# Kernel tuning notes

Measured on AMD Instinct MI355X. Metric: run time of the kernel, lower is better.

Reference implementation:

```python
import jax, jax.numpy as jnp
import numpy as np

NEG = -10000.0
START_ID, END_ID, PAD_ID = 0, 1, 2
B, S, T = 512, 512, 128


def setup_inputs() -> dict:
    key = jax.random.key(0)
    k1, k2, k3, k4 = jax.random.split(key, 4)
    x = jax.random.normal(k1, (B, S, T), dtype=jnp.float32)
    tags = jax.random.randint(k2, (B, S), 0, T)
    # prefix-ones mask; lengths in [1, S-2] so the gather at mask.sum(1) is in-range
    lengths = jax.random.randint(k3, (B,), 1, S - 1)
    mask = (jnp.arange(S)[None, :] < lengths[:, None]).astype(jnp.float32)
    # torch xavier_normal_ on (T, T): std = sqrt(2 / (T + T))
    std = (2.0 / (T + T)) ** 0.5
    transition = std * jax.random.normal(k4, (T, T), dtype=jnp.float32)
    return {"x": x, "tags": tags, "mask": mask, "transition": transition}


def _crf_forward(x, mask, transition):
    # forward algorithm: log partition function, shape (B,)
    b, s, t = x.shape
    alpha0 = jnp.full((b, t), NEG, dtype=x.dtype).at[:, START_ID].set(0.0)

    def step(alpha, inp):
        x_t, m_t = inp  # (B,T), (B,)
        # scores[b, next, prev] = alpha[b, prev] + x_t[b, next] + transition[next, prev]
        scores = alpha[:, None, :] + x_t[:, :, None] + transition[None, :, :]
        new = jax.scipy.special.logsumexp(scores, axis=2)  # (B,T)
        m = m_t[:, None]
        return new * m + alpha * (1.0 - m), None

    alpha, _ = jax.lax.scan(step, alpha0, (jnp.swapaxes(x, 0, 1), jnp.swapaxes(mask, 0, 1)))
    return jax.scipy.special.logsumexp(alpha + transition[END_ID], axis=1)


def _crf_score(x, tags, mask, transition):
    # gold path score, shape (B,) — emission at t is paired with tags[:, t+1]
    b, s, t = x.shape
    em = jnp.take_along_axis(x[:, : s - 1], tags[:, 1:s, None], axis=2)[..., 0]  # (B,S-1)
    tr = transition[tags[:, 1:s], tags[:, : s - 1]]  # (B,S-1)
    score = jnp.sum((em + tr) * mask[:, : s - 1], axis=1)
    last_idx = mask.sum(axis=1).astype(jnp.int32)  # (B,)
    last_tag = jnp.take_along_axis(tags, last_idx[:, None], axis=1)[:, 0]
    return score + transition[END_ID, last_tag]


def reference(x, tags, mask, transition):
    fwd_score = _crf_forward(x, mask, transition)
    gold_score = _crf_score(x, tags, mask, transition)
    return jnp.mean(fwd_score - gold_score)
```

## Files before the change

kernel.cpp:

```cpp
#include <hip/hip_runtime.h>

#define NTAG 128
#define SEQ 512
#define NBATCH 512
#define END_ID 1

typedef _Float16 h2 __attribute__((ext_vector_type(2)));
typedef __fp16 fp16x2 __attribute__((ext_vector_type(2)));
typedef uint u32x32 __attribute__((ext_vector_type(32)));

#define LOG2E 1.4426950408889634f
#define LN2   0.6931471805599453f

__device__ __forceinline__ float bcast0(float v) {
  return __int_as_float(__builtin_amdgcn_readfirstlane(__float_as_int(v)));
}
__device__ __forceinline__ uint pack2(float a, float b) {
  fp16x2 h = __builtin_amdgcn_cvt_pkrtz(a, b);
  return __builtin_bit_cast(uint, h);
}
__device__ __forceinline__ h2 as_h2(uint u) { return __builtin_bit_cast(h2, u); }

__device__ __forceinline__ float fast_exp2(float x) {
#if __has_builtin(__builtin_amdgcn_exp2f)
  return __builtin_amdgcn_exp2f(x);
#else
  return exp2f(x);
#endif
}
__device__ __forceinline__ float fast_log2(float x) {
#if __has_builtin(__builtin_amdgcn_logf)
  return __builtin_amdgcn_logf(x);
#else
  return log2f(x);
#endif
}

#if __has_builtin(__builtin_amdgcn_fdot2)
#define FDOT2(pu, eu, acc) acc = __builtin_amdgcn_fdot2(as_h2(pu), as_h2(eu), acc, false)
#else
#define FDOT2(pu, eu, acc) do { h2 _p = as_h2(pu), _e = as_h2(eu); \
  acc = fmaf((float)_p.x, (float)_e.x, fmaf((float)_p.y, (float)_e.y, acc)); } while (0)
#endif

#define RL(v, l) ((uint)__builtin_amdgcn_readlane((int)(v), (l)))
#define EL(c) ((c) < 32 ? eL0[(c)] : eL1[(c) - 32])
#define EH(c) ((c) < 32 ? eH0[(c)] : eH1[(c) - 32])

__global__ __launch_bounds__(64, 1) void crf_kernel(
    const float* __restrict__ x,
    const int*   __restrict__ tags,
    const float* __restrict__ mask,
    const float* __restrict__ trans,
    float* __restrict__ ws)
{
  const int b    = blockIdx.x;
  const int lane = threadIdx.x;

  const float* xb   = x    + (size_t)b * SEQ * NTAG;
  const float* mrow = mask + (size_t)b * SEQ;
  const int*   trow = tags + (size_t)b * SEQ;

  float msum = 0.f;
  #pragma unroll
  for (int i = 0; i < SEQ / 64; ++i) msum += mrow[lane + i * 64];
  #pragma unroll
  for (int off = 1; off < 64; off <<= 1) msum += __shfl_xor(msum, off);
  const int len = (int)msum;

  u32x32 eL0, eL1, eH0, eH1;
  {
    const float4* r0 = (const float4*)(trans + (size_t)(2 * lane) * NTAG);
    const float4* r1 = (const float4*)(trans + (size_t)(2 * lane + 1) * NTAG);
    #pragma unroll
    for (int k4 = 0; k4 < 16; ++k4) {
      float4 lo = r0[k4], hi = r1[k4];
      eL0[2 * k4 + 0] = pack2(fast_exp2(lo.x * LOG2E), fast_exp2(lo.y * LOG2E));
      eL0[2 * k4 + 1] = pack2(fast_exp2(lo.z * LOG2E), fast_exp2(lo.w * LOG2E));
      eH0[2 * k4 + 0] = pack2(fast_exp2(hi.x * LOG2E), fast_exp2(hi.y * LOG2E));
      eH0[2 * k4 + 1] = pack2(fast_exp2(hi.z * LOG2E), fast_exp2(hi.w * LOG2E));
    }
    #pragma unroll
    for (int k4 = 16; k4 < 32; ++k4) {
      float4 lo = r0[k4], hi = r1[k4];
      eL1[2 * (k4 - 16) + 0] = pack2(fast_exp2(lo.x * LOG2E), fast_exp2(lo.y * LOG2E));
      eL1[2 * (k4 - 16) + 1] = pack2(fast_exp2(lo.z * LOG2E), fast_exp2(lo.w * LOG2E));
      eH1[2 * (k4 - 16) + 0] = pack2(fast_exp2(hi.x * LOG2E), fast_exp2(hi.y * LOG2E));
      eH1[2 * (k4 - 16) + 1] = pack2(fast_exp2(hi.z * LOG2E), fast_exp2(hi.w * LOG2E));
    }
  }

  float A_lo = (lane == 0) ? 0.f : -14427.f;
  float A_hi = -14427.f;

  const float2* xrow = (const float2*)xb;
  float2 xf0 = xrow[0 * 64 + lane];
  float2 xf1 = xrow[1 * 64 + lane];
  float2 xf2 = xrow[2 * 64 + lane];
  float2 xf3 = xrow[3 * 64 + lane];

#define CRF_STEP(XF, S)                                                       \
  {                                                                           \
    const int g = t + (S);                                                    \
    const float M = bcast0(A_lo);                                             \
    const uint pk = pack2(fminf(fast_exp2(A_lo - M), 60000.f),                \
                          fminf(fast_exp2(A_hi - M), 60000.f));               \
    const float2 xt = XF;                                                     \
    XF = xrow[(size_t)min(g + 4, len) * 64 + lane];  \
    float qL0 = 0.f, qL1 = 0.f, qL2 = 0.f, qL3 = 0.f;                         \
    float qH0 = 0.f, qH1 = 0.f, qH2 = 0.f, qH3 = 0.f;                         \
    _Pragma("unroll")                                                         \
    for (int gg = 0; gg < 64; gg += 8) {                                      \
      const uint s0 = RL(pk, gg + 0), s1 = RL(pk, gg + 1);                    \
      const uint s2 = RL(pk, gg + 2), s3 = RL(pk, gg + 3);                    \
      const uint s4 = RL(pk, gg + 4), s5 = RL(pk, gg + 5);                    \
      const uint s6 = RL(pk, gg + 6), s7 = RL(pk, gg + 7);                    \
      FDOT2(s0, EL(gg + 0), qL0); FDOT2(s0, EH(gg + 0), qH0);                 \
      FDOT2(s1, EL(gg + 1), qL1); FDOT2(s1, EH(gg + 1), qH1);                 \
      FDOT2(s2, EL(gg + 2), qL2); FDOT2(s2, EH(gg + 2), qH2);                 \
      FDOT2(s3, EL(gg + 3), qL3); FDOT2(s3, EH(gg + 3), qH3);                 \
      FDOT2(s4, EL(gg + 4), qL0); FDOT2(s4, EH(gg + 4), qH0);                 \
      FDOT2(s5, EL(gg + 5), qL1); FDOT2(s5, EH(gg + 5), qH1);                 \
      FDOT2(s6, EL(gg + 6), qL2); FDOT2(s6, EH(gg + 6), qH2);                 \
      FDOT2(s7, EL(gg + 7), qL3); FDOT2(s7, EH(gg + 7), qH3);                 \
    }                                                                         \
    const float qL = (qL0 + qL1) + (qL2 + qL3);                               \
    const float qH = (qH0 + qH1) + (qH2 + qH3);                               \
    const float nL = fmaf(xt.x, LOG2E, M + fast_log2(qL));                    \
    const float nH = fmaf(xt.y, LOG2E, M + fast_log2(qH));                    \
    const bool act = (g < len);                                               \
    A_lo = act ? nL : A_lo;                                                   \
    A_hi = act ? nH : A_hi;                                                   \
  }

  for (int t = 0; t < len; t += 4) {
    CRF_STEP(xf0, 0)
    CRF_STEP(xf1, 1)
    CRF_STEP(xf2, 2)
    CRF_STEP(xf3, 3)
  }
#undef CRF_STEP

  const float a_lo = A_lo * LN2;
  const float a_hi = A_hi * LN2;

  const float2 te = ((const float2*)(trans + END_ID * NTAG))[lane];
  const float v_lo = a_lo + te.x;
  const float v_hi = a_hi + te.y;
  float m2 = fmaxf(v_lo, v_hi);
  #pragma unroll
  for (int off = 1; off < 64; off <<= 1) m2 = fmaxf(m2, __shfl_xor(m2, off));
  float s = fast_exp2((v_lo - m2) * LOG2E) + fast_exp2((v_hi - m2) * LOG2E);
  #pragma unroll
  for (int off = 1; off < 64; off <<= 1) s += __shfl_xor(s, off);
  const float fwd = m2 + fast_log2(s) * LN2;

  float g = 0.f;
  for (int i = lane; i < len; i += 64) {
    const int tn = trow[i + 1];
    const int tp = trow[i];
    g += xb[(size_t)i * NTAG + tn] + trans[tn * NTAG + tp];
  }
  #pragma unroll
  for (int off = 1; off < 64; off <<= 1) g += __shfl_xor(g, off);

  if (lane == 0) {
    const float gold = g + trans[END_ID * NTAG + trow[len]];
    ws[b] = fwd - gold;
  }
}

__global__ void reduce_kernel(const float* __restrict__ ws, float* __restrict__ out) {
  __shared__ float sm[8];
  const int tid = threadIdx.x;
  float v = ws[tid];
  #pragma unroll
  for (int off = 1; off < 64; off <<= 1) v += __shfl_xor(v, off);
  if ((tid & 63) == 0) sm[tid >> 6] = v;
  __syncthreads();
  if (tid == 0) {
    float s = 0.f;
    #pragma unroll
    for (int w = 0; w < 8; ++w) s += sm[w];
    out[0] = s * (1.0f / 512.0f);
  }
}

extern "C" void kernel_launch(void* const* d_in, const int* in_sizes, int n_in,
                              void* d_out, int out_size, void* d_ws, size_t ws_size,
                              hipStream_t stream) {
  const float* x     = (const float*)d_in[0];
  const int*   tags  = (const int*)d_in[1];
  const float* mask  = (const float*)d_in[2];
  const float* trans = (const float*)d_in[3];
  float*       ws    = (float*)d_ws;

  crf_kernel<<<NBATCH, 64, 0, stream>>>(x, tags, mask, trans, ws);
  reduce_kernel<<<1, 512, 0, stream>>>(ws, (float*)d_out);
}
```

Baseline: 389.3 us.

## Split CRF forward recursion across two waves with LDS exchange and linear-domain scaling

Result: slower. 465.6 us (+19.6%).

```diff
diff --git a/kernel.cpp b/kernel.cpp
--- a/kernel.cpp
+++ b/kernel.cpp
@@ -7,14 +7,10 @@
 
 typedef _Float16 h2 __attribute__((ext_vector_type(2)));
 typedef __fp16 fp16x2 __attribute__((ext_vector_type(2)));
-typedef uint u32x32 __attribute__((ext_vector_type(32)));
 
 #define LOG2E 1.4426950408889634f
 #define LN2   0.6931471805599453f
 
-__device__ __forceinline__ float bcast0(float v) {
-  return __int_as_float(__builtin_amdgcn_readfirstlane(__float_as_int(v)));
-}
 __device__ __forceinline__ uint pack2(float a, float b) {
   fp16x2 h = __builtin_amdgcn_cvt_pkrtz(a, b);
   return __builtin_bit_cast(uint, h);
@@ -44,18 +40,22 @@
 #endif
 
 #define RL(v, l) ((uint)__builtin_amdgcn_readlane((int)(v), (l)))
-#define EL(c) ((c) < 32 ? eL0[(c)] : eL1[(c) - 32])
-#define EH(c) ((c) < 32 ? eH0[(c)] : eH1[(c) - 32])
 
-__global__ __launch_bounds__(64, 1) void crf_kernel(
+__global__ __launch_bounds__(128) void crf_kernel(
     const float* __restrict__ x,
     const int*   __restrict__ tags,
     const float* __restrict__ mask,
     const float* __restrict__ trans,
     float* __restrict__ ws)
 {
-  const int b    = blockIdx.x;
-  const int lane = threadIdx.x;
+  const int b   = blockIdx.x;
+  const int tid = threadIdx.x;
+  const int w   = tid >> 6;
+  const int l   = tid & 63;
+  const int j   = (w << 6) + l;
+
+  __shared__ float pbuf[2][NTAG];
+  __shared__ float vbuf[NTAG];
 
   const float* xb   = x    + (size_t)b * SEQ * NTAG;
   const float* mrow = mask + (size_t)b * SEQ;
@@ -63,74 +63,65 @@
 
   float msum = 0.f;
   #pragma unroll
-  for (int i = 0; i < SEQ / 64; ++i) msum += mrow[lane + i * 64];
+  for (int i = 0; i < SEQ / 64; ++i) msum += mrow[l + i * 64];
   #pragma unroll
   for (int off = 1; off < 64; off <<= 1) msum += __shfl_xor(msum, off);
   const int len = (int)msum;
 
-  u32x32 eL0, eL1, eH0, eH1;
+  uint e[64];
   {
-    const float4* r0 = (const float4*)(trans + (size_t)(2 * lane) * NTAG);
-    const float4* r1 = (const float4*)(trans + (size_t)(2 * lane + 1) * NTAG);
+    const float4* tr = (const float4*)(trans + (size_t)j * NTAG);
     #pragma unroll
-    for (int k4 = 0; k4 < 16; ++k4) {
-      float4 lo = r0[k4], hi = r1[k4];
-      eL0[2 * k4 + 0] = pack2(fast_exp2(lo.x * LOG2E), fast_exp2(lo.y * LOG2E));
-      eL0[2 * k4 + 1] = pack2(fast_exp2(lo.z * LOG2E), fast_exp2(lo.w * LOG2E));
-      eH0[2 * k4 + 0] = pack2(fast_exp2(hi.x * LOG2E), fast_exp2(hi.y * LOG2E));
-      eH0[2 * k4 + 1] = pack2(fast_exp2(hi.z * LOG2E), fast_exp2(hi.w * LOG2E));
-    }
-    #pragma unroll
-    for (int k4 = 16; k4 < 32; ++k4) {
-      float4 lo = r0[k4], hi = r1[k4];
-      eL1[2 * (k4 - 16) + 0] = pack2(fast_exp2(lo.x * LOG2E), fast_exp2(lo.y * LOG2E));
-      eL1[2 * (k4 - 16) + 1] = pack2(fast_exp2(lo.z * LOG2E), fast_exp2(lo.w * LOG2E));
-      eH1[2 * (k4 - 16) + 0] = pack2(fast_exp2(hi.x * LOG2E), fast_exp2(hi.y * LOG2E));
-      eH1[2 * (k4 - 16) + 1] = pack2(fast_exp2(hi.z * LOG2E), fast_exp2(hi.w * LOG2E));
+    for (int k4 = 0; k4 < 32; ++k4) {
+      float4 t4 = tr[k4];
+      e[2 * k4 + 0] = pack2(fast_exp2(t4.x * LOG2E), fast_exp2(t4.y * LOG2E));
+      e[2 * k4 + 1] = pack2(fast_exp2(t4.z * LOG2E), fast_exp2(t4.w * LOG2E));
     }
   }
 
-  float A_lo = (lane == 0) ? 0.f : -14427.f;
-  float A_hi = -14427.f;
+  float pcur = (j == 0) ? 1.f : 0.f;
+  float M = 0.f;
+  pbuf[0][j] = pcur;
+  __syncthreads();
 
-  const float2* xrow = (const float2*)xb;
-  float2 xf0 = xrow[0 * 64 + lane];
-  float2 xf1 = xrow[1 * 64 + lane];
-  float2 xf2 = xrow[2 * 64 + lane];
-  float2 xf3 = xrow[3 * 64 + lane];
+  const float* xj = xb + j;
+  float xf0 = xj[0 * NTAG];
+  float xf1 = xj[1 * NTAG];
+  float xf2 = xj[2 * NTAG];
+  float xf3 = xj[3 * NTAG];
 
-#define CRF_STEP(XF, S)                                                       \
+#define CRF_STEP(XF, S_)                                                      \
   {                                                                           \
-    const int g = t + (S);                                                    \
-    const float M = bcast0(A_lo);                                             \
-    const uint pk = pack2(fminf(fast_exp2(A_lo - M), 60000.f),                \
-                          fminf(fast_exp2(A_hi - M), 60000.f));               \
-    const float2 xt = XF;                                                     \
-    XF = xrow[(size_t)min(g + 4, len) * 64 + lane];  \
-    float qL0 = 0.f, qL1 = 0.f, qL2 = 0.f, qL3 = 0.f;                         \
-    float qH0 = 0.f, qH1 = 0.f, qH2 = 0.f, qH3 = 0.f;                         \
+    const int g  = t + (S_);                                                  \
+    const int rs = (S_) & 1;                        \
+    const float exv = fast_exp2(XF * LOG2E);                  \
+    XF = xj[(size_t)min(g + 4, len) * NTAG];         \
+    const float2 pp = ((const float2*)pbuf[rs])[l];      \
+    const float  p0 = pbuf[rs][0];                        \
+    int c = ((__float_as_int(p0) >> 23) & 0xff) - 127;                        \
+    c = c < -60 ? -60 : (c > 60 ? 60 : c);                                    \
+    const float sc = __int_as_float((127 - c) << 23);             \
+    const uint pk = pack2(fminf(pp.x * sc, 60000.f),                          \
+                          fminf(pp.y * sc, 60000.f));                         \
+    float q0 = 0.f, q1 = 0.f, q2 = 0.f, q3 = 0.f;                             \
     _Pragma("unroll")                                                         \
     for (int gg = 0; gg < 64; gg += 8) {                                      \
       const uint s0 = RL(pk, gg + 0), s1 = RL(pk, gg + 1);                    \
       const uint s2 = RL(pk, gg + 2), s3 = RL(pk, gg + 3);                    \
       const uint s4 = RL(pk, gg + 4), s5 = RL(pk, gg + 5);                    \
       const uint s6 = RL(pk, gg + 6), s7 = RL(pk, gg + 7);                    \
-      FDOT2(s0, EL(gg + 0), qL0); FDOT2(s0, EH(gg + 0), qH0);                 \
-      FDOT2(s1, EL(gg + 1), qL1); FDOT2(s1, EH(gg + 1), qH1);                 \
-      FDOT2(s2, EL(gg + 2), qL2); FDOT2(s2, EH(gg + 2), qH2);                 \
-      FDOT2(s3, EL(gg + 3), qL3); FDOT2(s3, EH(gg + 3), qH3);                 \
-      FDOT2(s4, EL(gg + 4), qL0); FDOT2(s4, EH(gg + 4), qH0);                 \
-      FDOT2(s5, EL(gg + 5), qL1); FDOT2(s5, EH(gg + 5), qH1);                 \
-      FDOT2(s6, EL(gg + 6), qL2); FDOT2(s6, EH(gg + 6), qH2);                 \
-      FDOT2(s7, EL(gg + 7), qL3); FDOT2(s7, EH(gg + 7), qH3);                 \
+      FDOT2(s0, e[gg + 0], q0); FDOT2(s1, e[gg + 1], q1);                     \
+      FDOT2(s2, e[gg + 2], q2); FDOT2(s3, e[gg + 3], q3);                     \
+      FDOT2(s4, e[gg + 4], q0); FDOT2(s5, e[gg + 5], q1);                     \
+      FDOT2(s6, e[gg + 6], q2); FDOT2(s7, e[gg + 7], q3);                     \
     }                                                                         \
-    const float qL = (qL0 + qL1) + (qL2 + qL3);                               \
-    const float qH = (qH0 + qH1) + (qH2 + qH3);                               \
-    const float nL = fmaf(xt.x, LOG2E, M + fast_log2(qL));                    \
-    const float nH = fmaf(xt.y, LOG2E, M + fast_log2(qH));                    \
+    const float q  = (q0 + q1) + (q2 + q3);                                   \
+    const float pn = q * exv;                                                 \
     const bool act = (g < len);                                               \
-    A_lo = act ? nL : A_lo;                                                   \
-    A_hi = act ? nH : A_hi;                                                   \
+    pcur = act ? pn : pcur;                                                   \
+    M    = act ? (M + (float)c) : M;                                          \
+    pbuf[rs ^ 1][j] = pcur;                                                   \
+    __syncthreads();                                                          \
   }
 
   for (int t = 0; t < len; t += 4) {
@@ -141,32 +132,35 @@
   }
 #undef CRF_STEP
 
-  const float a_lo = A_lo * LN2;
-  const float a_hi = A_hi * LN2;
+  const float a_ln = (M + fast_log2(pcur)) * LN2;
+  vbuf[j] = a_ln;
+  __syncthreads();
 
-  const float2 te = ((const float2*)(trans + END_ID * NTAG))[lane];
-  const float v_lo = a_lo + te.x;
-  const float v_hi = a_hi + te.y;
-  float m2 = fmaxf(v_lo, v_hi);
-  #pragma unroll
-  for (int off = 1; off < 64; off <<= 1) m2 = fmaxf(m2, __shfl_xor(m2, off));
-  float s = fast_exp2((v_lo - m2) * LOG2E) + fast_exp2((v_hi - m2) * LOG2E);
-  #pragma unroll
-  for (int off = 1; off < 64; off <<= 1) s += __shfl_xor(s, off);
-  const float fwd = m2 + fast_log2(s) * LN2;
+  if (w == 0) {
+    const float2 te = ((const float2*)(trans + END_ID * NTAG))[l];
+    const float v_lo = vbuf[2 * l]     + te.x;
+    const float v_hi = vbuf[2 * l + 1] + te.y;
+    float m2 = fmaxf(v_lo, v_hi);
+    #pragma unroll
+    for (int off = 1; off < 64; off <<= 1) m2 = fmaxf(m2, __shfl_xor(m2, off));
+    float s = fast_exp2((v_lo - m2) * LOG2E) + fast_exp2((v_hi - m2) * LOG2E);
+    #pragma unroll
+    for (int off = 1; off < 64; off <<= 1) s += __shfl_xor(s, off);
+    const float fwd = m2 + fast_log2(s) * LN2;
 
-  float g = 0.f;
-  for (int i = lane; i < len; i += 64) {
-    const int tn = trow[i + 1];
-    const int tp = trow[i];
-    g += xb[(size_t)i * NTAG + tn] + trans[tn * NTAG + tp];
-  }
-  #pragma unroll
-  for (int off = 1; off < 64; off <<= 1) g += __shfl_xor(g, off);
+    float gacc = 0.f;
+    for (int i = l; i < len; i += 64) {
+      const int tn = trow[i + 1];
+      const int tp = trow[i];
+      gacc += xb[(size_t)i * NTAG + tn] + trans[tn * NTAG + tp];
+    }
+    #pragma unroll
+    for (int off = 1; off < 64; off <<= 1) gacc += __shfl_xor(gacc, off);
 
-  if (lane == 0) {
-    const float gold = g + trans[END_ID * NTAG + trow[len]];
-    ws[b] = fwd - gold;
+    if (l == 0) {
+      const float gold = gacc + trans[END_ID * NTAG + trow[len]];
+      ws[b] = fwd - gold;
+    }
   }
 }
 
@@ -195,6 +189,6 @@
   const float* trans = (const float*)d_in[3];
   float*       ws    = (float*)d_ws;
 
-  crf_kernel<<<NBATCH, 64, 0, stream>>>(x, tags, mask, trans, ws);
+  crf_kernel<<<NBATCH, 128, 0, stream>>>(x, tags, mask, trans, ws);
   reduce_kernel<<<1, 512, 0, stream>>>(ws, (float*)d_out);
 }
```

## Process two batch rows per wavefront to interleave independent recurrences

Applied to the files above, without the earlier changes.

Result: slower. 559.2 us (+43.7%).

```diff
diff --git a/kernel.cpp b/kernel.cpp
--- a/kernel.cpp
+++ b/kernel.cpp
@@ -4,6 +4,7 @@
 #define SEQ 512
 #define NBATCH 512
 #define END_ID 1
+#define NBPW 2
 
 typedef _Float16 h2 __attribute__((ext_vector_type(2)));
 typedef __fp16 fp16x2 __attribute__((ext_vector_type(2)));
@@ -46,6 +47,33 @@
 #define RL(v, l) ((uint)__builtin_amdgcn_readlane((int)(v), (l)))
 #define EL(c) ((c) < 32 ? eL0[(c)] : eL1[(c) - 32])
 #define EH(c) ((c) < 32 ? eH0[(c)] : eH1[(c) - 32])
+
+__device__ __forceinline__ float crf_tail(
+    float A_lo, float A_hi, int lane, const float* __restrict__ xb,
+    const int* __restrict__ trow, int len, const float* __restrict__ trans) {
+  const float a_lo = A_lo * LN2;
+  const float a_hi = A_hi * LN2;
+  const float2 te = ((const float2*)(trans + END_ID * NTAG))[lane];
+  const float v_lo = a_lo + te.x;
+  const float v_hi = a_hi + te.y;
+  float m2 = fmaxf(v_lo, v_hi);
+  #pragma unroll
+  for (int off = 1; off < 64; off <<= 1) m2 = fmaxf(m2, __shfl_xor(m2, off));
+  float s = fast_exp2((v_lo - m2) * LOG2E) + fast_exp2((v_hi - m2) * LOG2E);
+  #pragma unroll
+  for (int off = 1; off < 64; off <<= 1) s += __shfl_xor(s, off);
+  const float fwd = m2 + fast_log2(s) * LN2;
+
+  float g = 0.f;
+  for (int i = lane; i < len; i += 64) {
+    const int tn = trow[i + 1];
+    const int tp = trow[i];
+    g += xb[(size_t)i * NTAG + tn] + trans[(size_t)tn * NTAG + tp];
+  }
+  #pragma unroll
+  for (int off = 1; off < 64; off <<= 1) g += __shfl_xor(g, off);
+  return fwd - (g + trans[(size_t)END_ID * NTAG + trow[len]]);
+}
 
 __global__ __launch_bounds__(64, 1) void crf_kernel(
     const float* __restrict__ x,
@@ -54,19 +82,33 @@
     const float* __restrict__ trans,
     float* __restrict__ ws)
 {
-  const int b    = blockIdx.x;
+  const int b0   = blockIdx.x * NBPW;
+  const int b1   = b0 + 1;
   const int lane = threadIdx.x;
 
-  const float* xb   = x    + (size_t)b * SEQ * NTAG;
-  const float* mrow = mask + (size_t)b * SEQ;
-  const int*   trow = tags + (size_t)b * SEQ;
-
-  float msum = 0.f;
-  #pragma unroll
-  for (int i = 0; i < SEQ / 64; ++i) msum += mrow[lane + i * 64];
-  #pragma unroll
-  for (int off = 1; off < 64; off <<= 1) msum += __shfl_xor(msum, off);
-  const int len = (int)msum;
+  const float* xb0  = x + (size_t)b0 * SEQ * NTAG;
+  const float* xb1  = x + (size_t)b1 * SEQ * NTAG;
+  const int* trow0  = tags + (size_t)b0 * SEQ;
+  const int* trow1  = tags + (size_t)b1 * SEQ;
+
+  float ms0 = 0.f, ms1 = 0.f;
+  {
+    const float* mr0 = mask + (size_t)b0 * SEQ;
+    const float* mr1 = mask + (size_t)b1 * SEQ;
+    #pragma unroll
+    for (int i = 0; i < SEQ / 64; ++i) {
+      ms0 += mr0[lane + i * 64];
+      ms1 += mr1[lane + i * 64];
+    }
+    #pragma unroll
+    for (int off = 1; off < 64; off <<= 1) {
+      ms0 += __shfl_xor(ms0, off);
+      ms1 += __shfl_xor(ms1, off);
+    }
+  }
+  const int len0 = (int)ms0;
+  const int len1 = (int)ms1;
+  const int mlen = max(len0, len1);
 
   u32x32 eL0, eL1, eH0, eH1;
   {
@@ -90,83 +132,73 @@
     }
   }
 
-  float A_lo = (lane == 0) ? 0.f : -14427.f;
-  float A_hi = -14427.f;
-
-  const float2* xrow = (const float2*)xb;
-  float2 xf0 = xrow[0 * 64 + lane];
-  float2 xf1 = xrow[1 * 64 + lane];
-  float2 xf2 = xrow[2 * 64 + lane];
-  float2 xf3 = xrow[3 * 64 + lane];
-
-#define CRF_STEP(XF, S)                                                       \
+  float A0_lo = (lane == 0) ? 0.f : -14427.f;
+  float A0_hi = -14427.f;
+  float A1_lo = (lane == 0) ? 0.f : -14427.f;
+  float A1_hi = -14427.f;
+
+  const float2* xr0 = (const float2*)xb0;
+  const float2* xr1 = (const float2*)xb1;
+  float2 xa0 = xr0[0 * 64 + lane], xb_0 = xr1[0 * 64 + lane];
+  float2 xa1 = xr0[1 * 64 + lane], xb_1 = xr1[1 * 64 + lane];
+  float2 xa2 = xr0[2 * 64 + lane], xb_2 = xr1[2 * 64 + lane];
+  float2 xa3 = xr0[3 * 64 + lane], xb_3 = xr1[3 * 64 + lane];
+
+#define CRF_STEP2(XA, XB, S_)                                                 \
   {                                                                           \
-    const int g = t + (S);                                                    \
-    const float M = bcast0(A_lo);                                             \
-    const uint pk = pack2(fminf(fast_exp2(A_lo - M), 60000.f),                \
-                          fminf(fast_exp2(A_hi - M), 60000.f));               \
-    const float2 xt = XF;                                                     \
-    XF = xrow[(size_t)min(g + 4, len) * 64 + lane];  \
-    float qL0 = 0.f, qL1 = 0.f, qL2 = 0.f, qL3 = 0.f;                         \
-    float qH0 = 0.f, qH1 = 0.f, qH2 = 0.f, qH3 = 0.f;                         \
+    const int g = t + (S_);                                                   \
+    const float M0 = bcast0(A0_lo);                                           \
+    const float M1 = bcast0(A1_lo);                                           \
+    const uint pk0 = pack2(fminf(fast_exp2(A0_lo - M0), 60000.f),             \
+                           fminf(fast_exp2(A0_hi - M0), 60000.f));            \
+    const uint pk1 = pack2(fminf(fast_exp2(A1_lo - M1), 60000.f),             \
+                           fminf(fast_exp2(A1_hi - M1), 60000.f));            \
+    const float2 xt0 = XA;                                                    \
+    const float2 xt1 = XB;                                                    \
+    XA = xr0[(size_t)min(g + 4, len0) * 64 + lane];                           \
+    XB = xr1[(size_t)min(g + 4, len1) * 64 + lane];                           \
+    float q0L0 = 0.f, q0L1 = 0.f, q0H0 = 0.f, q0H1 = 0.f;                     \
+    float q1L0 = 0.f, q1L1 = 0.f, q1H0 = 0.f, q1H1 = 0.f;                     \
     _Pragma("unroll")                                                         \
-    for (int gg = 0; gg < 64; gg += 8) {                                      \
-      const uint s0 = RL(pk, gg + 0), s1 = RL(pk, gg + 1);                    \
-      const uint s2 = RL(pk, gg + 2), s3 = RL(pk, gg + 3);                    \
-      const uint s4 = RL(pk, gg + 4), s5 = RL(pk, gg + 5);                    \
-      const uint s6 = RL(pk, gg + 6), s7 = RL(pk, gg + 7);                    \
-      FDOT2(s0, EL(gg + 0), qL0); FDOT2(s0, EH(gg + 0), qH0);                 \
-      FDOT2(s1, EL(gg + 1), qL1); FDOT2(s1, EH(gg + 1), qH1);                 \
-      FDOT2(s2, EL(gg + 2), qL2); FDOT2(s2, EH(gg + 2), qH2);                 \
-      FDOT2(s3, EL(gg + 3), qL3); FDOT2(s3, EH(gg + 3), qH3);                 \
-      FDOT2(s4, EL(gg + 4), qL0); FDOT2(s4, EH(gg + 4), qH0);                 \
-      FDOT2(s5, EL(gg + 5), qL1); FDOT2(s5, EH(gg + 5), qH1);                 \
-      FDOT2(s6, EL(gg + 6), qL2); FDOT2(s6, EH(gg + 6), qH2);                 \
-      FDOT2(s7, EL(gg + 7), qL3); FDOT2(s7, EH(gg + 7), qH3);                 \
+    for (int gg = 0; gg < 64; gg += 4) {                                      \
+      const uint u0 = RL(pk0, gg + 0), w0 = RL(pk1, gg + 0);                  \
+      const uint u1 = RL(pk0, gg + 1), w1 = RL(pk1, gg + 1);                  \
+      const uint u2 = RL(pk0, gg + 2), w2 = RL(pk1, gg + 2);                  \
+      const uint u3 = RL(pk0, gg + 3), w3 = RL(pk1, gg + 3);                  \
+      FDOT2(u0, EL(gg + 0), q0L0); FDOT2(w0, EL(gg + 0), q1L0);               \
+      FDOT2(u0, EH(gg + 0), q0H0); FDOT2(w0, EH(gg + 0), q1H0);               \
+      FDOT2(u1, EL(gg + 1), q0L1); FDOT2(w1, EL(gg + 1), q1L1);               \
+      FDOT2(u1, EH(gg + 1), q0H1); FDOT2(w1, EH(gg + 1), q1H1);               \
+      FDOT2(u2, EL(gg + 2), q0L0); FDOT2(w2, EL(gg + 2), q1L0);               \
+      FDOT2(u2, EH(gg + 2), q0H0); FDOT2(w2, EH(gg + 2), q1H0);               \
+      FDOT2(u3, EL(gg + 3), q0L1); FDOT2(w3, EL(gg + 3), q1L1);               \
+      FDOT2(u3, EH(gg + 3), q0H1); FDOT2(w3, EH(gg + 3), q1H1);               \
     }                                                                         \
-    const float qL = (qL0 + qL1) + (qL2 + qL3);                               \
-    const float qH = (qH0 + qH1) + (qH2 + qH3);                               \
-    const float nL = fmaf(xt.x, LOG2E, M + fast_log2(qL));                    \
-    const float nH = fmaf(xt.y, LOG2E, M + fast_log2(qH));                    \
-    const bool act = (g < len);                                               \
-    A_lo = act ? nL : A_lo;                                                   \
-    A_hi = act ? nH : A_hi;                                                   \
-  }
-
-  for (int t = 0; t < len; t += 4) {
-    CRF_STEP(xf0, 0)
-    CRF_STEP(xf1, 1)
-    CRF_STEP(xf2, 2)
-    CRF_STEP(xf3, 3)
-  }
-#undef CRF_STEP
-
-  const float a_lo = A_lo * LN2;
-  const float a_hi = A_hi * LN2;
-
-  const float2 te = ((const float2*)(trans + END_ID * NTAG))[lane];
-  const float v_lo = a_lo + te.x;
-  const float v_hi = a_hi + te.y;
-  float m2 = fmaxf(v_lo, v_hi);
-  #pragma unroll
-  for (int off = 1; off < 64; off <<= 1) m2 = fmaxf(m2, __shfl_xor(m2, off));
-  float s = fast_exp2((v_lo - m2) * LOG2E) + fast_exp2((v_hi - m2) * LOG2E);
-  #pragma unroll
-  for (int off = 1; off < 64; off <<= 1) s += __shfl_xor(s, off);
-  const float fwd = m2 + fast_log2(s) * LN2;
-
-  float g = 0.f;
-  for (int i = lane; i < len; i += 64) {
-    const int tn = trow[i + 1];
-    const int tp = trow[i];
-    g += xb[(size_t)i * NTAG + tn] + trans[tn * NTAG + tp];
-  }
-  #pragma unroll
-  for (int off = 1; off < 64; off <<= 1) g += __shfl_xor(g, off);
-
+    const float q0L = q0L0 + q0L1, q0H = q0H0 + q0H1;                         \
+    const float q1L = q1L0 + q1L1, q1H = q1H0 + q1H1;                         \
+    const float n0L = fmaf(xt0.x, LOG2E, M0 + fast_log2(q0L));                \
+    const float n0H = fmaf(xt0.y, LOG2E, M0 + fast_log2(q0H));                \
+    const float n1L = fmaf(xt1.x, LOG2E, M1 + fast_log2(q1L));                \
+    const float n1H = fmaf(xt1.y, LOG2E, M1 + fast_log2(q1H));                \
+    const bool a0 = (g < len0);                                               \
+    const bool a1 = (g < len1);                                               \
+    A0_lo = a0 ? n0L : A0_lo;  A0_hi = a0 ? n0H : A0_hi;                      \
+    A1_lo = a1 ? n1L : A1_lo;  A1_hi = a1 ? n1H : A1_hi;                      \
+  }
+
+  for (int t = 0; t < mlen; t += 4) {
+    CRF_STEP2(xa0, xb_0, 0)
+    CRF_STEP2(xa1, xb_1, 1)
+    CRF_STEP2(xa2, xb_2, 2)
+    CRF_STEP2(xa3, xb_3, 3)
+  }
+#undef CRF_STEP2
+
+  const float r0v = crf_tail(A0_lo, A0_hi, lane, xb0, trow0, len0, trans);
+  const float r1v = crf_tail(A1_lo, A1_hi, lane, xb1, trow1, len1, trans);
   if (lane == 0) {
-    const float gold = g + trans[END_ID * NTAG + trow[len]];
-    ws[b] = fwd - gold;
+    ws[b0] = r0v;
+    ws[b1] = r1v;
   }
 }
 
@@ -195,6 +227,6 @@
   const float* trans = (const float*)d_in[3];
   float*       ws    = (float*)d_ws;
 
-  crf_kernel<<<NBATCH, 64, 0, stream>>>(x, tags, mask, trans, ws);
+  crf_kernel<<<NBATCH / NBPW, 64, 0, stream>>>(x, tags, mask, trans, ws);
   reduce_kernel<<<1, 512, 0, stream>>>(ws, (float*)d_out);
 }
```
